# Optimization experiments

Hardware: AMD Instinct MI355X
Metric: run time of the kernel (lower is better)

The kernel has to match this reference:

```python
import jax, jax.numpy as jnp
import numpy as np

N = 50000   # nodes
E = 800000  # edges (avg degree 16)
D = 2048    # resnet50 feature dim
C = 256     # layer_size
NEG_SLOPE = 0.2


def setup_inputs() -> dict:
    key = jax.random.key(0)
    ks = jax.random.split(key, 16)
    s = 0.02
    inp = {
        'x': jax.random.normal(ks[0], (N, D), jnp.float32),
        'edge_index': jax.random.randint(ks[1], (2, E), 0, N, dtype=jnp.int32),
        # GATConv layer 1 (in=D, out=C, heads=1)
        'W1': jax.random.normal(ks[2], (D, C), jnp.float32) * s,
        'a_src1': jax.random.normal(ks[3], (C,), jnp.float32) * s,
        'a_dst1': jax.random.normal(ks[4], (C,), jnp.float32) * s,
        'b1': jnp.zeros((C,), jnp.float32),
        # GATConv layer 2 (in=C, out=C)
        'W2': jax.random.normal(ks[5], (C, C), jnp.float32) * s,
        'a_src2': jax.random.normal(ks[6], (C,), jnp.float32) * s,
        'a_dst2': jax.random.normal(ks[7], (C,), jnp.float32) * s,
        'b2': jnp.zeros((C,), jnp.float32),
        # EdgePredictor: lin1 (2C -> C), lin2 (C -> 1)
        'Wp1': jax.random.normal(ks[8], (2 * C, C), jnp.float32) * s,
        'bp1': jnp.zeros((C,), jnp.float32),
        'wp2': jax.random.normal(ks[9], (C,), jnp.float32) * s,
        'bp2': jnp.zeros((), jnp.float32),
    }
    return inp


def gat_layer(x, src, dst, W, a_src, a_dst, b, n_nodes):
    # PyG GATConv, heads=1, concat=True: message flows src -> dst,
    # softmax over incoming edges of each dst node.
    h = x @ W                                   # [N, C]
    e = jax.nn.leaky_relu((h @ a_src)[src] + (h @ a_dst)[dst], NEG_SLOPE)  # [E]
    emax = jax.ops.segment_max(e, dst, num_segments=n_nodes)
    ex = jnp.exp(e - emax[dst])
    denom = jax.ops.segment_sum(ex, dst, num_segments=n_nodes)
    alpha = ex / (denom[dst] + 1e-16)           # [E]
    out = jax.ops.segment_sum(h[src] * alpha[:, None], dst, num_segments=n_nodes)
    return out + b


def reference(x, edge_index, W1, a_src1, a_dst1, b1, W2, a_src2, a_dst2, b2,
              Wp1, bp1, wp2, bp2):
    src, dst = edge_index[0], edge_index[1]
    # GATConv default add_self_loops=True
    loops = jnp.arange(N, dtype=src.dtype)
    src_sl = jnp.concatenate([src, loops])
    dst_sl = jnp.concatenate([dst, loops])

    h = gat_layer(x, src_sl, dst_sl, W1, a_src1, a_dst1, b1, N)
    h = gat_layer(h, src_sl, dst_sl, W2, a_src2, a_dst2, b2, N)

    # edge predictor on the ORIGINAL edge_index (no self loops)
    xe = jnp.concatenate([h[src], h[dst]], axis=-1)       # [E, 2C]
    z = jax.nn.relu(xe @ Wp1 + bp1)                        # [E, C]  (dropout: eval mode)
    return z @ wp2 + bp2                                   # [E]
```

## Files before the change

kernel.cpp:

```cpp
#include <hip/hip_runtime.h>
#include <hip/hip_bf16.h>
#include <stdint.h>

#define NNODES 50000
#define NEDGES 800000
#define DIN    2048
#define CDIM   256
#define ELOOP  (NEDGES + NNODES)

using bf16x8 = __attribute__((ext_vector_type(8))) short;
using f32x4  = __attribute__((ext_vector_type(4))) float;
using gvoid  = __attribute__((address_space(1))) const void;
using lvoid  = __attribute__((address_space(3))) void;

__device__ __forceinline__ float bf2f(uint16_t u) {
    union { uint32_t i; float f; } v; v.i = (uint32_t)u << 16; return v.f;
}
__device__ __forceinline__ uint16_t f2bf(float f) {
    union { float f; uint32_t i; } v; v.f = f;
    uint32_t i = v.i;
    return (uint16_t)((i + 0x7FFFu + ((i >> 16) & 1u)) >> 16);
}

#define BM 128
#define BN 128
#define BK 32

__global__ __launch_bounds__(256)
void gemm_bt(const uint16_t* __restrict__ A, const uint16_t* __restrict__ Bt,
             uint16_t* __restrict__ C, const float* __restrict__ bias,
             int M, int N, int K)
{
    __shared__ __align__(16) uint16_t lA[BM * BK];
    __shared__ __align__(16) uint16_t lB[BN * BK];
    const int tid  = threadIdx.x;
    const int wave = tid >> 6;
    const int lane = tid & 63;
    const int lm = lane & 15, lq = lane >> 4;
    const int bm = blockIdx.x * BM;
    const int bn = blockIdx.y * BN;
    const int wm = (wave >> 1) * 64;
    const int wn = (wave & 1) * 64;

    f32x4 acc[4][4];
    for (int i = 0; i < 4; ++i)
        for (int j = 0; j < 4; ++j)
            acc[i][j] = (f32x4)0.0f;

    for (int k0 = 0; k0 < K; k0 += BK) {
        for (int j = 0; j < 2; ++j) {
            int c = j * 256 + wave * 64 + lane;
            int row = c >> 2, cc = c & 3;
            int gr = bm + row; if (gr >= M) gr = M - 1;
            const uint16_t* gp = A + (size_t)gr * K + k0 + cc * 8;
            __builtin_amdgcn_global_load_lds((gvoid*)gp,
                (lvoid*)(lA + (size_t)(j * 256 + wave * 64) * 8), 16, 0, 0);
        }
        for (int j = 0; j < 2; ++j) {
            int c = j * 256 + wave * 64 + lane;
            int row = c >> 2, cc = c & 3;
            int gr = bn + row; if (gr >= N) gr = N - 1;
            const uint16_t* gp = Bt + (size_t)gr * K + k0 + cc * 8;
            __builtin_amdgcn_global_load_lds((gvoid*)gp,
                (lvoid*)(lB + (size_t)(j * 256 + wave * 64) * 8), 16, 0, 0);
        }
        __syncthreads();

        bf16x8 af[4], bfr[4];
        for (int mt = 0; mt < 4; ++mt)
            af[mt] = *(const bf16x8*)(lA + (wm + mt * 16 + lm) * BK + lq * 8);
        for (int nt = 0; nt < 4; ++nt)
            bfr[nt] = *(const bf16x8*)(lB + (wn + nt * 16 + lm) * BK + lq * 8);

        for (int mt = 0; mt < 4; ++mt)
            for (int nt = 0; nt < 4; ++nt)
                acc[mt][nt] = __builtin_amdgcn_mfma_f32_16x16x32_bf16(
                    af[mt], bfr[nt], acc[mt][nt], 0, 0, 0);
        __syncthreads();
    }

    for (int mt = 0; mt < 4; ++mt) {
        for (int nt = 0; nt < 4; ++nt) {
            int gn = bn + wn + nt * 16 + lm;
            float badd = bias ? bias[gn] : 0.0f;
            for (int r = 0; r < 4; ++r) {
                int gm = bm + wm + mt * 16 + lq * 4 + r;
                if (gm < M)
                    C[(size_t)gm * N + gn] = f2bf(acc[mt][nt][r] + badd);
            }
        }
    }
}

__global__ __launch_bounds__(256)
void gemm_f32_bt(const float* __restrict__ A, const uint16_t* __restrict__ Bt,
                 uint16_t* __restrict__ C, int M, int N, int K)
{
    __shared__ __align__(16) float    lA[BM * BK];
    __shared__ __align__(16) uint16_t lB[BN * BK];
    const int tid  = threadIdx.x;
    const int wave = tid >> 6;
    const int lane = tid & 63;
    const int lm = lane & 15, lq = lane >> 4;
    const int bm = blockIdx.x * BM;
    const int bn = blockIdx.y * BN;
    const int wm = (wave >> 1) * 64;
    const int wn = (wave & 1) * 64;

    f32x4 acc[4][4];
    for (int i = 0; i < 4; ++i)
        for (int j = 0; j < 4; ++j)
            acc[i][j] = (f32x4)0.0f;

    for (int k0 = 0; k0 < K; k0 += BK) {
        for (int j = 0; j < 4; ++j) {
            int c = j * 256 + wave * 64 + lane;
            int row = c >> 3;
            int lc  = (c & 7) ^ (row & 7);
            int gr = bm + row; if (gr >= M) gr = M - 1;
            const float* gp = A + (size_t)gr * K + k0 + lc * 4;
            __builtin_amdgcn_global_load_lds((gvoid*)gp,
                (lvoid*)(lA + (size_t)(j * 256 + wave * 64) * 4), 16, 0, 0);
        }
        for (int j = 0; j < 2; ++j) {
            int c = j * 256 + wave * 64 + lane;
            int row = c >> 2, cc = c & 3;
            const uint16_t* gp = Bt + (size_t)(bn + row) * K + k0 + cc * 8;
            __builtin_amdgcn_global_load_lds((gvoid*)gp,
                (lvoid*)(lB + (size_t)(j * 256 + wave * 64) * 8), 16, 0, 0);
        }
        __syncthreads();

        bf16x8 af[4], bfr[4];
        for (int mt = 0; mt < 4; ++mt) {
            int r = wm + mt * 16 + lm;
            int s0 = (lq * 2)     ^ (r & 7);
            int s1 = (lq * 2 + 1) ^ (r & 7);
            f32x4 a0 = *(const f32x4*)(lA + r * BK + s0 * 4);
            f32x4 a1 = *(const f32x4*)(lA + r * BK + s1 * 4);
            bf16x8 t;
            for (int q = 0; q < 4; ++q) {
                t[q]     = (short)f2bf(a0[q]);
                t[q + 4] = (short)f2bf(a1[q]);
            }
            af[mt] = t;
        }
        for (int nt = 0; nt < 4; ++nt)
            bfr[nt] = *(const bf16x8*)(lB + (wn + nt * 16 + lm) * BK + lq * 8);

        for (int mt = 0; mt < 4; ++mt)
            for (int nt = 0; nt < 4; ++nt)
                acc[mt][nt] = __builtin_amdgcn_mfma_f32_16x16x32_bf16(
                    af[mt], bfr[nt], acc[mt][nt], 0, 0, 0);
        __syncthreads();
    }

    for (int mt = 0; mt < 4; ++mt) {
        for (int nt = 0; nt < 4; ++nt) {
            int gn = bn + wn + nt * 16 + lm;
            for (int r = 0; r < 4; ++r) {
                int gm = bm + wm + mt * 16 + lq * 4 + r;
                if (gm < M)
                    C[(size_t)gm * N + gn] = f2bf(acc[mt][nt][r]);
            }
        }
    }
}

__global__ void transpose_cvt_kernel(const float* __restrict__ W,
                                     uint16_t* __restrict__ Wt, int K, int N)
{
    int idx = blockIdx.x * 256 + threadIdx.x;
    if (idx >= K * N) return;
    int n = idx / K, k = idx - n * K;
    Wt[idx] = f2bf(W[(size_t)k * N + n]);
}

__global__ void count_kernel(const int* __restrict__ ei, int* __restrict__ rs)
{
    int i = blockIdx.x * 256 + threadIdx.x;
    if (i >= ELOOP) return;
    int dst = (i < NEDGES) ? ei[NEDGES + i] : (i - NEDGES);
    atomicAdd(&rs[dst + 1], 1);
}

__global__ __launch_bounds__(1024)
void scan_kernel(int* __restrict__ rs, int* __restrict__ cursor)
{
    __shared__ int wsum[16];
    const int tid = threadIdx.x, lane = tid & 63, w = tid >> 6;
    int carry = 0;
    for (int base = 0; base <= NNODES; base += 1024) {
        int i = base + tid;
        int v = (i <= NNODES) ? rs[i] : 0;
        int s = v;
        for (int d = 1; d < 64; d <<= 1) {
            int t = __shfl_up(s, d);
            if (lane >= d) s += t;
        }
        if (lane == 63) wsum[w] = s;
        __syncthreads();
        if (tid < 16) {
            int x = wsum[tid];
            for (int d = 1; d < 16; d <<= 1) {
                int t = __shfl_up(x, d);
                if (tid >= d) x += t;
            }
            wsum[tid] = x;
        }
        __syncthreads();
        int incl = s + carry + (w > 0 ? wsum[w - 1] : 0);
        if (i <= NNODES) {
            rs[i] = incl;
            if (i < NNODES) cursor[i] = incl;
        }
        int total = carry + wsum[15];
        __syncthreads();
        carry = total;
    }
}

__global__ void fill_kernel(const int* __restrict__ ei, int* __restrict__ cursor,
                            int* __restrict__ csr_src)
{
    int i = blockIdx.x * 256 + threadIdx.x;
    if (i >= ELOOP) return;
    int src, dst;
    if (i < NEDGES) { src = ei[i]; dst = ei[NEDGES + i]; }
    else            { src = dst = i - NEDGES; }
    int pos = atomicAdd(&cursor[dst], 1);
    csr_src[pos] = src;
}

__global__ __launch_bounds__(256)
void rowdot_kernel(const uint16_t* __restrict__ g,
                   const float* __restrict__ asrc,
                   const float* __restrict__ adst,
                   float* __restrict__ s_src, float* __restrict__ s_dst)
{
    int n = blockIdx.x * 4 + (threadIdx.x >> 6);
    int lane = threadIdx.x & 63;
    ushort4 rv = *(const ushort4*)(g + (size_t)n * CDIM + lane * 4);
    float4 av = *(const float4*)(asrc + lane * 4);
    float4 dv = *(const float4*)(adst + lane * 4);
    float r0 = bf2f(rv.x), r1 = bf2f(rv.y), r2 = bf2f(rv.z), r3 = bf2f(rv.w);
    float a = r0 * av.x + r1 * av.y + r2 * av.z + r3 * av.w;
    float b = r0 * dv.x + r1 * dv.y + r2 * dv.z + r3 * dv.w;
    for (int d = 32; d; d >>= 1) { a += __shfl_xor(a, d); b += __shfl_xor(b, d); }
    if (lane == 0) { s_src[n] = a; s_dst[n] = b; }
}

__global__ __launch_bounds__(256)
void attn_kernel(const int* __restrict__ row_start, const int* __restrict__ csr_src,
                 const float* __restrict__ s_src, const float* __restrict__ s_dst,
                 const uint16_t* __restrict__ g, const float* __restrict__ bvec,
                 uint16_t* __restrict__ hout)
{
    int n = blockIdx.x * 4 + (threadIdx.x >> 6);
    int lane = threadIdx.x & 63;
    int beg = row_start[n], end = row_start[n + 1];
    float sdn = s_dst[n];

    float m = -1e30f;
    for (int i = beg + lane; i < end; i += 64) {
        float e = s_src[csr_src[i]] + sdn;
        e = (e > 0.f) ? e : 0.2f * e;
        m = fmaxf(m, e);
    }
    for (int d = 32; d; d >>= 1) m = fmaxf(m, __shfl_xor(m, d));

    float sum = 0.f;
    for (int i = beg + lane; i < end; i += 64) {
        float e = s_src[csr_src[i]] + sdn;
        e = (e > 0.f) ? e : 0.2f * e;
        sum += __expf(e - m);
    }
    for (int d = 32; d; d >>= 1) sum += __shfl_xor(sum, d);
    float inv = 1.f / (sum + 1e-16f);

    float a0 = 0.f, a1 = 0.f, a2 = 0.f, a3 = 0.f;
    for (int i = beg; i < end; ++i) {
        int src = csr_src[i];
        float e = s_src[src] + sdn;
        e = (e > 0.f) ? e : 0.2f * e;
        float alpha = __expf(e - m) * inv;
        ushort4 rv = *(const ushort4*)(g + (size_t)src * CDIM + lane * 4);
        a0 += alpha * bf2f(rv.x);
        a1 += alpha * bf2f(rv.y);
        a2 += alpha * bf2f(rv.z);
        a3 += alpha * bf2f(rv.w);
    }
    float4 bv = *(const float4*)(bvec + lane * 4);
    ushort4 o;
    o.x = f2bf(a0 + bv.x);
    o.y = f2bf(a1 + bv.y);
    o.z = f2bf(a2 + bv.z);
    o.w = f2bf(a3 + bv.w);
    *(ushort4*)(hout + (size_t)n * CDIM + lane * 4) = o;
}

__global__ __launch_bounds__(256)
void edgepred_kernel(const int* __restrict__ ei,
                     const uint16_t* __restrict__ U, const uint16_t* __restrict__ V,
                     const float* __restrict__ wp2, const float* __restrict__ bp2,
                     float* __restrict__ out)
{
    const int tid = threadIdx.x;
    const int grp = tid >> 4, l = tid & 15;
    const int e = blockIdx.x * 16 + grp;
    int src = ei[e];
    int dst = ei[NEDGES + e];
    const uint4 u0 = *(const uint4*)(U + (size_t)src * CDIM + l * 16);
    const uint4 u1 = *(const uint4*)(U + (size_t)src * CDIM + l * 16 + 8);
    const uint4 v0 = *(const uint4*)(V + (size_t)dst * CDIM + l * 16);
    const uint4 v1 = *(const uint4*)(V + (size_t)dst * CDIM + l * 16 + 8);
    const float4 w0 = *(const float4*)(wp2 + l * 16);
    const float4 w1 = *(const float4*)(wp2 + l * 16 + 4);
    const float4 w2 = *(const float4*)(wp2 + l * 16 + 8);
    const float4 w3 = *(const float4*)(wp2 + l * 16 + 12);
    float acc = 0.f;
    auto proc = [&](uint32_t uu, uint32_t vv, float wa, float wb) {
        float z0 = fmaxf(bf2f((uint16_t)(uu & 0xffffu)) + bf2f((uint16_t)(vv & 0xffffu)), 0.f);
        float z1 = fmaxf(bf2f((uint16_t)(uu >> 16)) + bf2f((uint16_t)(vv >> 16)), 0.f);
        acc += z0 * wa + z1 * wb;
    };
    proc(u0.x, v0.x, w0.x, w0.y); proc(u0.y, v0.y, w0.z, w0.w);
    proc(u0.z, v0.z, w1.x, w1.y); proc(u0.w, v0.w, w1.z, w1.w);
    proc(u1.x, v1.x, w2.x, w2.y); proc(u1.y, v1.y, w2.z, w2.w);
    proc(u1.z, v1.z, w3.x, w3.y); proc(u1.w, v1.w, w3.z, w3.w);
    for (int d = 1; d < 16; d <<= 1) acc += __shfl_xor(acc, d);
    if (l == 0) out[e] = acc + *bp2;
}

extern "C" void kernel_launch(void* const* d_in, const int* in_sizes, int n_in,
                              void* d_out, int out_size, void* d_ws, size_t ws_size,
                              hipStream_t stream)
{
    const float* x   = (const float*)d_in[0];
    const int*   ei  = (const int*)d_in[1];
    const float* W1  = (const float*)d_in[2];
    const float* as1 = (const float*)d_in[3];
    const float* ad1 = (const float*)d_in[4];
    const float* b1  = (const float*)d_in[5];
    const float* W2  = (const float*)d_in[6];
    const float* as2 = (const float*)d_in[7];
    const float* ad2 = (const float*)d_in[8];
    const float* b2  = (const float*)d_in[9];
    const float* Wp1 = (const float*)d_in[10];
    const float* bp1 = (const float*)d_in[11];
    const float* wp2 = (const float*)d_in[12];
    const float* bp2 = (const float*)d_in[13];
    float* out = (float*)d_out;

    char* ws = (char*)d_ws;
    size_t off = 0;
    auto alloc = [&](size_t bytes) -> void* {
        void* p = ws + off;
        off += (bytes + 255) & ~(size_t)255;
        return p;
    };
    uint16_t* W1t  = (uint16_t*)alloc((size_t)DIN * CDIM * 2);
    uint16_t* W2t  = (uint16_t*)alloc((size_t)CDIM * CDIM * 2);
    uint16_t* WpAt = (uint16_t*)alloc((size_t)CDIM * CDIM * 2);
    uint16_t* WpBt = (uint16_t*)alloc((size_t)CDIM * CDIM * 2);
    int* row_start = (int*)alloc((NNODES + 1) * sizeof(int));
    int* cursor    = (int*)alloc(NNODES * sizeof(int));
    int* csr_src   = (int*)alloc((size_t)ELOOP * sizeof(int));
    float* s_src   = (float*)alloc(NNODES * sizeof(float));
    float* s_dst   = (float*)alloc(NNODES * sizeof(float));
    uint16_t* G    = (uint16_t*)alloc((size_t)NNODES * CDIM * 2);
    uint16_t* H    = (uint16_t*)alloc((size_t)NNODES * CDIM * 2);
    uint16_t* Vb   = (uint16_t*)alloc((size_t)NNODES * CDIM * 2);

    hipMemsetAsync(row_start, 0, (NNODES + 1) * sizeof(int), stream);

    transpose_cvt_kernel<<<(DIN * CDIM + 255) / 256, 256, 0, stream>>>(W1, W1t, DIN, CDIM);
    transpose_cvt_kernel<<<(CDIM * CDIM + 255) / 256, 256, 0, stream>>>(W2, W2t, CDIM, CDIM);
    transpose_cvt_kernel<<<(CDIM * CDIM + 255) / 256, 256, 0, stream>>>(Wp1, WpAt, CDIM, CDIM);
    transpose_cvt_kernel<<<(CDIM * CDIM + 255) / 256, 256, 0, stream>>>(Wp1 + CDIM * CDIM, WpBt, CDIM, CDIM);

    count_kernel<<<(ELOOP + 255) / 256, 256, 0, stream>>>(ei, row_start);
    scan_kernel<<<1, 1024, 0, stream>>>(row_start, cursor);
    fill_kernel<<<(ELOOP + 255) / 256, 256, 0, stream>>>(ei, cursor, csr_src);

    dim3 gg((NNODES + BM - 1) / BM, CDIM / BN);

    gemm_f32_bt<<<gg, 256, 0, stream>>>(x, W1t, G, NNODES, CDIM, DIN);
    rowdot_kernel<<<NNODES / 4, 256, 0, stream>>>(G, as1, ad1, s_src, s_dst);
    attn_kernel<<<NNODES / 4, 256, 0, stream>>>(row_start, csr_src, s_src, s_dst, G, b1, H);

    gemm_bt<<<gg, 256, 0, stream>>>(H, W2t, G, nullptr, NNODES, CDIM, CDIM);
    rowdot_kernel<<<NNODES / 4, 256, 0, stream>>>(G, as2, ad2, s_src, s_dst);
    attn_kernel<<<NNODES / 4, 256, 0, stream>>>(row_start, csr_src, s_src, s_dst, G, b2, H);

    gemm_bt<<<gg, 256, 0, stream>>>(H, WpAt, G, bp1, NNODES, CDIM, CDIM);
    gemm_bt<<<gg, 256, 0, stream>>>(H, WpBt, Vb, nullptr, NNODES, CDIM, CDIM);

    edgepred_kernel<<<NEDGES / 16, 256, 0, stream>>>(ei, G, Vb, wp2, bp2, out);
}
```

Baseline: 1.244 ms.

## Reshape layer-1 GEMM tile, merge predictor GEMMs, traverse edges via CSR

The first GEMM now uses 64x256 tiles, so each block covers all output columns and reads each fp32 row of x only once instead of once per column block. The two edge-predictor GEMMs become one GEMM with N=512 writing an interleaved UV buffer, with a padded bias vector. The edge predictor now walks the CSR grouped by destination, loading the dst half once per node and scattering results through a new per-edge id array. The costs are an extra csr_eid array, divergent self-loop skips, and serial per-node edge loops with uneven degree.

```diff
diff --git a/kernel.cpp b/kernel.cpp
--- a/kernel.cpp
+++ b/kernel.cpp
@@ -92,20 +92,21 @@
     }
 }
 
+#define FM 64
+#define FN 256
+
 __global__ __launch_bounds__(256)
 void gemm_f32_bt(const float* __restrict__ A, const uint16_t* __restrict__ Bt,
-                 uint16_t* __restrict__ C, int M, int N, int K)
-{
-    __shared__ __align__(16) float    lA[BM * BK];
-    __shared__ __align__(16) uint16_t lB[BN * BK];
+                 uint16_t* __restrict__ C, int M, int K)
+{
+    __shared__ __align__(16) float    lA[FM * BK];
+    __shared__ __align__(16) uint16_t lB[FN * BK];
     const int tid  = threadIdx.x;
     const int wave = tid >> 6;
     const int lane = tid & 63;
     const int lm = lane & 15, lq = lane >> 4;
-    const int bm = blockIdx.x * BM;
-    const int bn = blockIdx.y * BN;
-    const int wm = (wave >> 1) * 64;
-    const int wn = (wave & 1) * 64;
+    const int bm = blockIdx.x * FM;
+    const int wn = wave * 64;
 
     f32x4 acc[4][4];
     for (int i = 0; i < 4; ++i)
@@ -113,7 +114,7 @@
             acc[i][j] = (f32x4)0.0f;
 
     for (int k0 = 0; k0 < K; k0 += BK) {
-        for (int j = 0; j < 4; ++j) {
+        for (int j = 0; j < 2; ++j) {
             int c = j * 256 + wave * 64 + lane;
             int row = c >> 3;
             int lc  = (c & 7) ^ (row & 7);
@@ -122,10 +123,10 @@
             __builtin_amdgcn_global_load_lds((gvoid*)gp,
                 (lvoid*)(lA + (size_t)(j * 256 + wave * 64) * 4), 16, 0, 0);
         }
-        for (int j = 0; j < 2; ++j) {
+        for (int j = 0; j < 4; ++j) {
             int c = j * 256 + wave * 64 + lane;
             int row = c >> 2, cc = c & 3;
-            const uint16_t* gp = Bt + (size_t)(bn + row) * K + k0 + cc * 8;
+            const uint16_t* gp = Bt + (size_t)row * K + k0 + cc * 8;
             __builtin_amdgcn_global_load_lds((gvoid*)gp,
                 (lvoid*)(lB + (size_t)(j * 256 + wave * 64) * 8), 16, 0, 0);
         }
@@ -133,7 +134,7 @@
 
         bf16x8 af[4], bfr[4];
         for (int mt = 0; mt < 4; ++mt) {
-            int r = wm + mt * 16 + lm;
+            int r = mt * 16 + lm;
             int s0 = (lq * 2)     ^ (r & 7);
             int s1 = (lq * 2 + 1) ^ (r & 7);
             f32x4 a0 = *(const f32x4*)(lA + r * BK + s0 * 4);
@@ -157,11 +158,11 @@
 
     for (int mt = 0; mt < 4; ++mt) {
         for (int nt = 0; nt < 4; ++nt) {
-            int gn = bn + wn + nt * 16 + lm;
+            int gn = wn + nt * 16 + lm;
             for (int r = 0; r < 4; ++r) {
-                int gm = bm + wm + mt * 16 + lq * 4 + r;
+                int gm = bm + mt * 16 + lq * 4 + r;
                 if (gm < M)
-                    C[(size_t)gm * N + gn] = f2bf(acc[mt][nt][r]);
+                    C[(size_t)gm * FN + gn] = f2bf(acc[mt][nt][r]);
             }
         }
     }
@@ -174,6 +175,12 @@
     if (idx >= K * N) return;
     int n = idx / K, k = idx - n * K;
     Wt[idx] = f2bf(W[(size_t)k * N + n]);
+}
+
+__global__ void bias512_kernel(const float* __restrict__ bp1, float* __restrict__ b512)
+{
+    int i = threadIdx.x + blockIdx.x * 256;
+    if (i < 512) b512[i] = (i < CDIM) ? bp1[i] : 0.0f;
 }
 
 __global__ void count_kernel(const int* __restrict__ ei, int* __restrict__ rs)
@@ -221,15 +228,16 @@
 }
 
 __global__ void fill_kernel(const int* __restrict__ ei, int* __restrict__ cursor,
-                            int* __restrict__ csr_src)
+                            int* __restrict__ csr_src, int* __restrict__ csr_eid)
 {
     int i = blockIdx.x * 256 + threadIdx.x;
     if (i >= ELOOP) return;
-    int src, dst;
-    if (i < NEDGES) { src = ei[i]; dst = ei[NEDGES + i]; }
-    else            { src = dst = i - NEDGES; }
+    int src, dst, eid;
+    if (i < NEDGES) { src = ei[i]; dst = ei[NEDGES + i]; eid = i; }
+    else            { src = dst = i - NEDGES; eid = -1; }
     int pos = atomicAdd(&cursor[dst], 1);
     csr_src[pos] = src;
+    csr_eid[pos] = eid;
 }
 
 __global__ __launch_bounds__(256)
@@ -300,36 +308,33 @@
 }
 
 __global__ __launch_bounds__(256)
-void edgepred_kernel(const int* __restrict__ ei,
-                     const uint16_t* __restrict__ U, const uint16_t* __restrict__ V,
+void edgepred_kernel(const int* __restrict__ row_start, const int* __restrict__ csr_src,
+                     const int* __restrict__ csr_eid,
+                     const uint16_t* __restrict__ UV,
                      const float* __restrict__ wp2, const float* __restrict__ bp2,
                      float* __restrict__ out)
 {
-    const int tid = threadIdx.x;
-    const int grp = tid >> 4, l = tid & 15;
-    const int e = blockIdx.x * 16 + grp;
-    int src = ei[e];
-    int dst = ei[NEDGES + e];
-    const uint4 u0 = *(const uint4*)(U + (size_t)src * CDIM + l * 16);
-    const uint4 u1 = *(const uint4*)(U + (size_t)src * CDIM + l * 16 + 8);
-    const uint4 v0 = *(const uint4*)(V + (size_t)dst * CDIM + l * 16);
-    const uint4 v1 = *(const uint4*)(V + (size_t)dst * CDIM + l * 16 + 8);
-    const float4 w0 = *(const float4*)(wp2 + l * 16);
-    const float4 w1 = *(const float4*)(wp2 + l * 16 + 4);
-    const float4 w2 = *(const float4*)(wp2 + l * 16 + 8);
-    const float4 w3 = *(const float4*)(wp2 + l * 16 + 12);
-    float acc = 0.f;
-    auto proc = [&](uint32_t uu, uint32_t vv, float wa, float wb) {
-        float z0 = fmaxf(bf2f((uint16_t)(uu & 0xffffu)) + bf2f((uint16_t)(vv & 0xffffu)), 0.f);
-        float z1 = fmaxf(bf2f((uint16_t)(uu >> 16)) + bf2f((uint16_t)(vv >> 16)), 0.f);
-        acc += z0 * wa + z1 * wb;
-    };
-    proc(u0.x, v0.x, w0.x, w0.y); proc(u0.y, v0.y, w0.z, w0.w);
-    proc(u0.z, v0.z, w1.x, w1.y); proc(u0.w, v0.w, w1.z, w1.w);
-    proc(u1.x, v1.x, w2.x, w2.y); proc(u1.y, v1.y, w2.z, w2.w);
-    proc(u1.z, v1.z, w3.x, w3.y); proc(u1.w, v1.w, w3.z, w3.w);
-    for (int d = 1; d < 16; d <<= 1) acc += __shfl_xor(acc, d);
-    if (l == 0) out[e] = acc + *bp2;
+    int n = blockIdx.x * 4 + (threadIdx.x >> 6);
+    int lane = threadIdx.x & 63;
+    int beg = row_start[n], end = row_start[n + 1];
+
+    ushort4 vv = *(const ushort4*)(UV + (size_t)n * 512 + 256 + lane * 4);
+    float v0 = bf2f(vv.x), v1 = bf2f(vv.y), v2 = bf2f(vv.z), v3 = bf2f(vv.w);
+    float4 w = *(const float4*)(wp2 + lane * 4);
+    float bias = *bp2;
+
+    for (int i = beg; i < end; ++i) {
+        int eid = csr_eid[i];
+        if (eid < 0) continue;
+        int src = csr_src[i];
+        ushort4 uu = *(const ushort4*)(UV + (size_t)src * 512 + lane * 4);
+        float acc = fmaxf(bf2f(uu.x) + v0, 0.f) * w.x
+                  + fmaxf(bf2f(uu.y) + v1, 0.f) * w.y
+                  + fmaxf(bf2f(uu.z) + v2, 0.f) * w.z
+                  + fmaxf(bf2f(uu.w) + v3, 0.f) * w.w;
+        for (int d = 32; d; d >>= 1) acc += __shfl_xor(acc, d);
+        if (lane == 0) out[eid] = acc + bias;
+    }
 }
 
 extern "C" void kernel_launch(void* const* d_in, const int* in_sizes, int n_in,
@@ -361,40 +366,43 @@
     };
     uint16_t* W1t  = (uint16_t*)alloc((size_t)DIN * CDIM * 2);
     uint16_t* W2t  = (uint16_t*)alloc((size_t)CDIM * CDIM * 2);
-    uint16_t* WpAt = (uint16_t*)alloc((size_t)CDIM * CDIM * 2);
-    uint16_t* WpBt = (uint16_t*)alloc((size_t)CDIM * CDIM * 2);
+    uint16_t* WpCt = (uint16_t*)alloc((size_t)512 * CDIM * 2);
+    float* bias512 = (float*)alloc(512 * sizeof(float));
     int* row_start = (int*)alloc((NNODES + 1) * sizeof(int));
     int* cursor    = (int*)alloc(NNODES * sizeof(int));
     int* csr_src   = (int*)alloc((size_t)ELOOP * sizeof(int));
+    int* csr_eid   = (int*)alloc((size_t)ELOOP * sizeof(int));
     float* s_src   = (float*)alloc(NNODES * sizeof(float));
     float* s_dst   = (float*)alloc(NNODES * sizeof(float));
     uint16_t* G    = (uint16_t*)alloc((size_t)NNODES * CDIM * 2);
     uint16_t* H    = (uint16_t*)alloc((size_t)NNODES * CDIM * 2);
-    uint16_t* Vb   = (uint16_t*)alloc((size_t)NNODES * CDIM * 2);
+    uint16_t* UV   = (uint16_t*)alloc((size_t)NNODES * 512 * 2);
 
     hipMemsetAsync(row_start, 0, (NNODES + 1) * sizeof(int), stream);
 
     transpose_cvt_kernel<<<(DIN * CDIM + 255) / 256, 256, 0, stream>>>(W1, W1t, DIN, CDIM);
     transpose_cvt_kernel<<<(CDIM * CDIM + 255) / 256, 256, 0, stream>>>(W2, W2t, CDIM, CDIM);
-    transpose_cvt_kernel<<<(CDIM * CDIM + 255) / 256, 256, 0, stream>>>(Wp1, WpAt, CDIM, CDIM);
-    transpose_cvt_kernel<<<(CDIM * CDIM + 255) / 256, 256, 0, stream>>>(Wp1 + CDIM * CDIM, WpBt, CDIM, CDIM);
+    transpose_cvt_kernel<<<(CDIM * CDIM + 255) / 256, 256, 0, stream>>>(Wp1, WpCt, CDIM, CDIM);
+    transpose_cvt_kernel<<<(CDIM * CDIM + 255) / 256, 256, 0, stream>>>(Wp1 + CDIM * CDIM,
+                                                                        WpCt + CDIM * CDIM, CDIM, CDIM);
+    bias512_kernel<<<2, 256, 0, stream>>>(bp1, bias512);
 
     count_kernel<<<(ELOOP + 255) / 256, 256, 0, stream>>>(ei, row_start);
     scan_kernel<<<1, 1024, 0, stream>>>(row_start, cursor);
-    fill_kernel<<<(ELOOP + 255) / 256, 256, 0, stream>>>(ei, cursor, csr_src);
-
-    dim3 gg((NNODES + BM - 1) / BM, CDIM / BN);
-
-    gemm_f32_bt<<<gg, 256, 0, stream>>>(x, W1t, G, NNODES, CDIM, DIN);
+    fill_kernel<<<(ELOOP + 255) / 256, 256, 0, stream>>>(ei, cursor, csr_src, csr_eid);
+
+    gemm_f32_bt<<<(NNODES + FM - 1) / FM, 256, 0, stream>>>(x, W1t, G, NNODES, DIN);
     rowdot_kernel<<<NNODES / 4, 256, 0, stream>>>(G, as1, ad1, s_src, s_dst);
     attn_kernel<<<NNODES / 4, 256, 0, stream>>>(row_start, csr_src, s_src, s_dst, G, b1, H);
 
-    gemm_bt<<<gg, 256, 0, stream>>>(H, W2t, G, nullptr, NNODES, CDIM, CDIM);
+    dim3 g2((NNODES + BM - 1) / BM, CDIM / BN);
+    gemm_bt<<<g2, 256, 0, stream>>>(H, W2t, G, nullptr, NNODES, CDIM, CDIM);
     rowdot_kernel<<<NNODES / 4, 256, 0, stream>>>(G, as2, ad2, s_src, s_dst);
     attn_kernel<<<NNODES / 4, 256, 0, stream>>>(row_start, csr_src, s_src, s_dst, G, b2, H);
 
-    gemm_bt<<<gg, 256, 0, stream>>>(H, WpAt, G, bp1, NNODES, CDIM, CDIM);
-    gemm_bt<<<gg, 256, 0, stream>>>(H, WpBt, Vb, nullptr, NNODES, CDIM, CDIM);
-
-    edgepred_kernel<<<NEDGES / 16, 256, 0, stream>>>(ei, G, Vb, wp2, bp2, out);
-}
+    dim3 g3((NNODES + BM - 1) / BM, 512 / BN);
+    gemm_bt<<<g3, 256, 0, stream>>>(H, WpCt, UV, bias512, NNODES, 512, CDIM);
+
+    edgepred_kernel<<<NNODES / 4, 256, 0, stream>>>(row_start, csr_src, csr_eid,
+                                                    UV, wp2, bp2, out);
+}
```

Result: no change. 1.259 ms (+1.2%).
